# Kernel tuning notes

Hardware: AMD Instinct MI355X
Metric: run time of the kernel (lower is better)

The kernel has to match this reference:

```python
import jax, jax.numpy as jnp
import numpy as np
from jax.ops import segment_sum

N_V = 50000   # vertices
N_E = 10000   # hyperedges
N_P = 800000  # incidence pairs
D_IN = 256
D_OUT = 256
NEG_SLOPE = 0.01


def setup_inputs() -> dict:
    key = jax.random.key(0)
    k1, k2, k3, k4, k5 = jax.random.split(key, 5)
    X = jax.random.normal(k1, (N_V, D_IN), dtype=jnp.float32)
    W = jax.random.normal(k2, (D_IN, D_OUT), dtype=jnp.float32) * (1.0 / np.sqrt(D_IN))
    b = jax.random.normal(k3, (D_OUT,), dtype=jnp.float32) * 0.01
    v_idx = jax.random.randint(k4, (N_P,), 0, N_V, dtype=jnp.int32)
    e_idx = jax.random.randint(k5, (N_P,), 0, N_E, dtype=jnp.int32)
    return {"X": X, "W": W, "b": b, "v_idx": v_idx, "e_idx": e_idx,
            "num_hyperedges": N_E}


def _mean_scatter(msg, idx, num_segments):
    # segment mean with count clamped to >=1 (empty segments -> 0)
    s = segment_sum(msg, idx, num_segments=num_segments)
    cnt = segment_sum(jnp.ones((msg.shape[0],), msg.dtype), idx,
                      num_segments=num_segments)
    return s / jnp.maximum(cnt, 1.0)[:, None]


def reference(X, W, b, v_idx, e_idx, num_hyperedges):
    # theta: linear projection  [N_V, D_OUT]
    H = X @ W + b
    # v2e mean: hyperedge features from member vertices
    e_feat = _mean_scatter(H[v_idx], e_idx, num_hyperedges)   # [N_E, D_OUT]
    # e2v mean: vertex features from incident hyperedges
    v_feat = _mean_scatter(e_feat[e_idx], v_idx, X.shape[0])  # [N_V, D_OUT]
    # leaky relu, default negative slope 0.01
    return jnp.where(v_feat >= 0, v_feat, NEG_SLOPE * v_feat)
```

## Files before the change

kernel.cpp:

```cpp
#include <hip/hip_runtime.h>

#define D 256
#define NEG_SLOPE 0.01f
#define E_PAD 192
#define V_PAD 64
#define EB 32
#define VB 64
#define NBE 313
#define NBV 782
#define CAP_E 3328
#define CAP_V 1536
#define CHUNK 4096
#define NS 8
#define DS 32

__device__ __forceinline__ unsigned short f2bf(float f) {
    union { float f; unsigned u; } x; x.f = f;
    unsigned r = x.u + 0x7fffu + ((x.u >> 16) & 1u);
    return (unsigned short)(r >> 16);
}
__device__ __forceinline__ float bf2f(unsigned short h) {
    union { float f; unsigned u; } x; x.u = ((unsigned)h) << 16;
    return x.f;
}

__global__ __launch_bounds__(256) void prep_kernel(
        const float* __restrict__ X, unsigned short* __restrict__ Xhs,
        const int* __restrict__ v_idx, const int* __restrict__ e_idx,
        int* __restrict__ bc_e, int* __restrict__ bc_v,
        unsigned* __restrict__ pe, unsigned* __restrict__ pv,
        int n_v, int n_p, int gp) {
    __shared__ int he[NBE], hv[NBV], beb[NBE], bvb[NBV];
    const int tid = threadIdx.x;
    if ((int)blockIdx.x < gp) {
        const int base = (int)blockIdx.x * CHUNK;
        for (int i = tid; i < NBE; i += 256) he[i] = 0;
        for (int i = tid; i < NBV; i += 256) hv[i] = 0;
        __syncthreads();
        #pragma unroll 4
        for (int r = 0; r < CHUNK / 256; ++r) {
            int p = base + r * 256 + tid;
            if (p < n_p) {
                atomicAdd(&he[e_idx[p] >> 5], 1);
                atomicAdd(&hv[v_idx[p] >> 6], 1);
            }
        }
        __syncthreads();
        for (int b = tid; b < NBE; b += 256) {
            int c = he[b];
            beb[b] = c ? atomicAdd(&bc_e[b], c) : 0;
            he[b] = 0;
        }
        for (int b = tid; b < NBV; b += 256) {
            int c = hv[b];
            bvb[b] = c ? atomicAdd(&bc_v[b], c) : 0;
            hv[b] = 0;
        }
        __syncthreads();
        #pragma unroll 4
        for (int r = 0; r < CHUNK / 256; ++r) {
            int p = base + r * 256 + tid;
            if (p < n_p) {
                int e = e_idx[p], v = v_idx[p];
                int b1 = e >> 5;
                int s1 = beb[b1] + atomicAdd(&he[b1], 1);
                if (s1 < CAP_E) pe[(size_t)b1 * CAP_E + s1] = (unsigned)v | ((unsigned)e << 16);
                int b2 = v >> 6;
                int s2 = bvb[b2] + atomicAdd(&hv[b2], 1);
                if (s2 < CAP_V) pv[(size_t)b2 * CAP_V + s2] = (unsigned)e | ((unsigned)v << 16);
            }
        }
    } else {
        int i = ((int)blockIdx.x - gp) * 256 + tid;
        if (i >= n_v * 64) return;
        int v = i >> 6;
        int d4 = (i & 63) * 4;
        float4 val = *(const float4*)(X + (size_t)v * D + d4);
        ushort4 h;
        h.x = f2bf(val.x); h.y = f2bf(val.y); h.z = f2bf(val.z); h.w = f2bf(val.w);
        int s = d4 >> 5, wd = d4 & 31;
        *(ushort4*)(Xhs + (size_t)s * n_v * DS + (size_t)v * DS + wd) = h;
    }
}

__global__ __launch_bounds__(256) void build_kernel(
        const unsigned* __restrict__ pe, const unsigned* __restrict__ pv,
        const int* __restrict__ bc_e, const int* __restrict__ bc_v,
        unsigned short* __restrict__ e_adj, int* __restrict__ e_fill,
        unsigned short* __restrict__ v_adj, int* __restrict__ v_fill,
        int n_e, int n_v) {
    __shared__ unsigned short adj[EB * E_PAD];
    __shared__ int cnt[VB];
    const int tid = threadIdx.x;
    if ((int)blockIdx.x < NBE) {
        const int b = blockIdx.x;
        const int e0 = b * EB;
        int m = n_e - e0; if (m > EB) m = EB;
        for (int i = tid; i < EB; i += 256) cnt[i] = 0;
        __syncthreads();
        int total = bc_e[b]; if (total > CAP_E) total = CAP_E;
        for (int i = tid; i < total; i += 256) {
            unsigned p = pe[(size_t)b * CAP_E + i];
            int v = (int)(p & 0xFFFFu);
            int el = (int)(p >> 16) - e0;
            int s = atomicAdd(&cnt[el], 1);
            if (s < E_PAD) adj[el * E_PAD + s] = (unsigned short)v;
        }
        __syncthreads();
        unsigned* gout = (unsigned*)(e_adj + (size_t)e0 * E_PAD);
        const unsigned* lin = (const unsigned*)adj;
        int words = m * E_PAD / 2;
        for (int j = tid; j < words; j += 256) gout[j] = lin[j];
        for (int el = tid; el < m; el += 256) {
            int c = cnt[el]; if (c > E_PAD) c = E_PAD;
            e_fill[e0 + el] = c;
        }
    } else {
        const int b = (int)blockIdx.x - NBE;
        const int v0 = b * VB;
        int m = n_v - v0; if (m > VB) m = VB;
        for (int i = tid; i < VB; i += 256) cnt[i] = 0;
        __syncthreads();
        int total = bc_v[b]; if (total > CAP_V) total = CAP_V;
        for (int i = tid; i < total; i += 256) {
            unsigned p = pv[(size_t)b * CAP_V + i];
            int e = (int)(p & 0xFFFFu);
            int vl = (int)(p >> 16) - v0;
            int s = atomicAdd(&cnt[vl], 1);
            if (s < V_PAD) adj[vl * V_PAD + s] = (unsigned short)e;
        }
        __syncthreads();
        unsigned* gout = (unsigned*)(v_adj + (size_t)v0 * V_PAD);
        const unsigned* lin = (const unsigned*)adj;
        int words = m * V_PAD / 2;
        for (int j = tid; j < words; j += 256) gout[j] = lin[j];
        for (int vl = tid; vl < m; vl += 256) {
            int c = cnt[vl]; if (c > V_PAD) c = V_PAD;
            v_fill[v0 + vl] = c;
        }
    }
}

__global__ __launch_bounds__(256) void v2e_kernel(
        const unsigned short* __restrict__ Xhs, const int* __restrict__ e_fill,
        const unsigned short* __restrict__ e_adj, float* __restrict__ Xagg,
        int n_e, int n_v) {
    const int s   = blockIdx.x;
    const int grp = threadIdx.x >> 3;
    const int sub = threadIdx.x & 7;
    const int e   = blockIdx.y * 32 + grp;
    if (e >= n_e) return;
    const unsigned short* tab = Xhs + (size_t)s * n_v * DS + (sub << 2);
    const unsigned short* adj = e_adj + (size_t)e * E_PAD;
    int cnt = e_fill[e]; if (cnt > E_PAD) cnt = E_PAD;
    float ax = 0.f, ay = 0.f, az = 0.f, aw = 0.f;
    int i = 0;
    for (; i + 8 <= cnt; i += 8) {
        ushort4 A0 = *(const ushort4*)(adj + i);
        ushort4 A1 = *(const ushort4*)(adj + i + 4);
        ushort4 a0 = *(const ushort4*)(tab + (size_t)A0.x * DS);
        ushort4 a1 = *(const ushort4*)(tab + (size_t)A0.y * DS);
        ushort4 a2 = *(const ushort4*)(tab + (size_t)A0.z * DS);
        ushort4 a3 = *(const ushort4*)(tab + (size_t)A0.w * DS);
        ushort4 a4 = *(const ushort4*)(tab + (size_t)A1.x * DS);
        ushort4 a5 = *(const ushort4*)(tab + (size_t)A1.y * DS);
        ushort4 a6 = *(const ushort4*)(tab + (size_t)A1.z * DS);
        ushort4 a7 = *(const ushort4*)(tab + (size_t)A1.w * DS);
        ax += (bf2f(a0.x) + bf2f(a1.x)) + (bf2f(a2.x) + bf2f(a3.x))
            + (bf2f(a4.x) + bf2f(a5.x)) + (bf2f(a6.x) + bf2f(a7.x));
        ay += (bf2f(a0.y) + bf2f(a1.y)) + (bf2f(a2.y) + bf2f(a3.y))
            + (bf2f(a4.y) + bf2f(a5.y)) + (bf2f(a6.y) + bf2f(a7.y));
        az += (bf2f(a0.z) + bf2f(a1.z)) + (bf2f(a2.z) + bf2f(a3.z))
            + (bf2f(a4.z) + bf2f(a5.z)) + (bf2f(a6.z) + bf2f(a7.z));
        aw += (bf2f(a0.w) + bf2f(a1.w)) + (bf2f(a2.w) + bf2f(a3.w))
            + (bf2f(a4.w) + bf2f(a5.w)) + (bf2f(a6.w) + bf2f(a7.w));
    }
    for (; i < cnt; ++i) {
        int v = adj[i];
        ushort4 a = *(const ushort4*)(tab + (size_t)v * DS);
        ax += bf2f(a.x); ay += bf2f(a.y); az += bf2f(a.z); aw += bf2f(a.w);
    }
    int c = cnt < 1 ? 1 : cnt;
    float inv = 1.0f / (float)c;
    float4 o;
    o.x = ax * inv; o.y = ay * inv; o.z = az * inv; o.w = aw * inv;
    *(float4*)(Xagg + (size_t)e * D + s * DS + (sub << 2)) = o;
}

#define BM 64
#define BN 64
#define BK 64
#define SAK 68
#define SBN 68

__global__ __launch_bounds__(256) void gemm_kernel(
        const float* __restrict__ A, const float* __restrict__ B,
        const float* __restrict__ bias, const int* __restrict__ e_cnt,
        unsigned short* __restrict__ Ehs, int M) {
    __shared__ float As[BM * SAK];
    __shared__ float Bs[BK * SBN];
    const int tid = threadIdx.x;
    const int tx = tid & 15, ty = tid >> 4;
    const int m0 = blockIdx.y * BM;
    const int n0 = blockIdx.x * BN;

    float acc[4][4] = {};

    for (int k0 = 0; k0 < D; k0 += BK) {
        #pragma unroll
        for (int r = 0; r < 4; ++r) {
            int l  = (tid + r * 256) * 4;
            int am = l >> 6;
            int ak = l & 63;
            int grow = m0 + am;
            float4 v = make_float4(0.f, 0.f, 0.f, 0.f);
            if (grow < M) v = *(const float4*)(A + (size_t)grow * D + k0 + ak);
            *(float4*)(&As[am * SAK + ak]) = v;
        }
        #pragma unroll
        for (int r = 0; r < 4; ++r) {
            int l  = (tid + r * 256) * 4;
            int bk = l >> 6;
            int bn = l & 63;
            float4 v = *(const float4*)(B + (size_t)(k0 + bk) * D + n0 + bn);
            *(float4*)(&Bs[bk * SBN + bn]) = v;
        }
        __syncthreads();

        #pragma unroll 8
        for (int kk = 0; kk < BK; ++kk) {
            float a0 = As[(ty * 4 + 0) * SAK + kk];
            float a1 = As[(ty * 4 + 1) * SAK + kk];
            float a2 = As[(ty * 4 + 2) * SAK + kk];
            float a3 = As[(ty * 4 + 3) * SAK + kk];
            float4 bv = *(const float4*)(Bs + kk * SBN + tx * 4);
            acc[0][0] += a0 * bv.x; acc[0][1] += a0 * bv.y; acc[0][2] += a0 * bv.z; acc[0][3] += a0 * bv.w;
            acc[1][0] += a1 * bv.x; acc[1][1] += a1 * bv.y; acc[1][2] += a1 * bv.z; acc[1][3] += a1 * bv.w;
            acc[2][0] += a2 * bv.x; acc[2][1] += a2 * bv.y; acc[2][2] += a2 * bv.z; acc[2][3] += a2 * bv.w;
            acc[3][0] += a3 * bv.x; acc[3][1] += a3 * bv.y; acc[3][2] += a3 * bv.z; acc[3][3] += a3 * bv.w;
        }
        __syncthreads();
    }

    float4 bb = *(const float4*)(bias + n0 + tx * 4);
    const int dcol = n0 + tx * 4;
    const int ss = dcol >> 5, wd = dcol & 31;
    #pragma unroll
    for (int i = 0; i < 4; ++i) {
        int row = m0 + ty * 4 + i;
        if (row < M) {
            bool nonempty = e_cnt[row] > 0;
            ushort4 o;
            o.x = f2bf(nonempty ? acc[i][0] + bb.x : 0.f);
            o.y = f2bf(nonempty ? acc[i][1] + bb.y : 0.f);
            o.z = f2bf(nonempty ? acc[i][2] + bb.z : 0.f);
            o.w = f2bf(nonempty ? acc[i][3] + bb.w : 0.f);
            *(ushort4*)(Ehs + (size_t)ss * M * DS + (size_t)row * DS + wd) = o;
        }
    }
}

__global__ __launch_bounds__(256) void e2v_kernel(
        const unsigned short* __restrict__ Ehs, const unsigned short* __restrict__ v_adj,
        const int* __restrict__ v_fill, float* __restrict__ out, int n_v, int n_e) {
    const int s   = blockIdx.x;
    const int grp = threadIdx.x >> 3;
    const int sub = threadIdx.x & 7;
    const int v   = blockIdx.y * 32 + grp;
    if (v >= n_v) return;
    const unsigned short* tab = Ehs + (size_t)s * n_e * DS + (sub << 2);
    const unsigned short* a = v_adj + (size_t)v * V_PAD;
    int c = v_fill[v]; if (c > V_PAD) c = V_PAD;
    float ax = 0.f, ay = 0.f, az = 0.f, aw = 0.f;
    int i = 0;
    for (; i + 8 <= c; i += 8) {
        ushort4 E0 = *(const ushort4*)(a + i);
        ushort4 E1 = *(const ushort4*)(a + i + 4);
        ushort4 a0 = *(const ushort4*)(tab + (size_t)E0.x * DS);
        ushort4 a1 = *(const ushort4*)(tab + (size_t)E0.y * DS);
        ushort4 a2 = *(const ushort4*)(tab + (size_t)E0.z * DS);
        ushort4 a3 = *(const ushort4*)(tab + (size_t)E0.w * DS);
        ushort4 a4 = *(const ushort4*)(tab + (size_t)E1.x * DS);
        ushort4 a5 = *(const ushort4*)(tab + (size_t)E1.y * DS);
        ushort4 a6 = *(const ushort4*)(tab + (size_t)E1.z * DS);
        ushort4 a7 = *(const ushort4*)(tab + (size_t)E1.w * DS);
        ax += (bf2f(a0.x) + bf2f(a1.x)) + (bf2f(a2.x) + bf2f(a3.x))
            + (bf2f(a4.x) + bf2f(a5.x)) + (bf2f(a6.x) + bf2f(a7.x));
        ay += (bf2f(a0.y) + bf2f(a1.y)) + (bf2f(a2.y) + bf2f(a3.y))
            + (bf2f(a4.y) + bf2f(a5.y)) + (bf2f(a6.y) + bf2f(a7.y));
        az += (bf2f(a0.z) + bf2f(a1.z)) + (bf2f(a2.z) + bf2f(a3.z))
            + (bf2f(a4.z) + bf2f(a5.z)) + (bf2f(a6.z) + bf2f(a7.z));
        aw += (bf2f(a0.w) + bf2f(a1.w)) + (bf2f(a2.w) + bf2f(a3.w))
            + (bf2f(a4.w) + bf2f(a5.w)) + (bf2f(a6.w) + bf2f(a7.w));
    }
    for (; i < c; ++i) {
        int e = a[i];
        ushort4 x = *(const ushort4*)(tab + (size_t)e * DS);
        ax += bf2f(x.x); ay += bf2f(x.y); az += bf2f(x.z); aw += bf2f(x.w);
    }
    int cc = c < 1 ? 1 : c;
    float inv = 1.0f / (float)cc;
    ax *= inv; ay *= inv; az *= inv; aw *= inv;
    float4 o;
    o.x = ax >= 0.f ? ax : NEG_SLOPE * ax;
    o.y = ay >= 0.f ? ay : NEG_SLOPE * ay;
    o.z = az >= 0.f ? az : NEG_SLOPE * az;
    o.w = aw >= 0.f ? aw : NEG_SLOPE * aw;
    *(float4*)(out + (size_t)v * D + s * DS + (sub << 2)) = o;
}

extern "C" void kernel_launch(void* const* d_in, const int* in_sizes, int n_in,
                              void* d_out, int out_size, void* d_ws, size_t ws_size,
                              hipStream_t stream) {
    const float* X    = (const float*)d_in[0];
    const float* W    = (const float*)d_in[1];
    const float* bias = (const float*)d_in[2];
    const int* v_idx  = (const int*)d_in[3];
    const int* e_idx  = (const int*)d_in[4];
    const int n_v = in_sizes[0] / D;
    const int n_p = in_sizes[3];
    const int n_e = 10000;

    char* w = (char*)d_ws;
    size_t off = 0;
    auto alloc = [&](size_t bytes) -> void* {
        void* p = w + off;
        off = (off + bytes + 255) & ~(size_t)255;
        return p;
    };
    unsigned short* Xhs = (unsigned short*)alloc((size_t)NS * n_v * DS * sizeof(unsigned short));
    float* Xagg         = (float*)alloc((size_t)n_e * D * sizeof(float));
    unsigned short* Ehs = (unsigned short*)alloc((size_t)n_e * D * sizeof(unsigned short));
    unsigned short* e_adj = (unsigned short*)alloc((size_t)n_e * E_PAD * sizeof(unsigned short));
    unsigned short* v_adj = (unsigned short*)alloc((size_t)n_v * V_PAD * sizeof(unsigned short));
    unsigned* pe   = (unsigned*)alloc((size_t)NBE * CAP_E * sizeof(unsigned));
    unsigned* pv   = (unsigned*)alloc((size_t)NBV * CAP_V * sizeof(unsigned));
    int* fills     = (int*)alloc((size_t)(n_e + n_v) * sizeof(int));
    int* e_fill = fills;
    int* v_fill = fills + n_e;
    int* bc        = (int*)alloc((size_t)(NBE + NBV) * sizeof(int));
    int* bc_e = bc;
    int* bc_v = bc + NBE;

    hipMemsetAsync(bc, 0, (size_t)(NBE + NBV) * sizeof(int), stream);

    int gp = (n_p + CHUNK - 1) / CHUNK;
    int gc = (n_v * 64 + 255) / 256;
    prep_kernel<<<gp + gc, 256, 0, stream>>>(X, Xhs, v_idx, e_idx,
                                             bc_e, bc_v, pe, pv, n_v, n_p, gp);

    build_kernel<<<NBE + NBV, 256, 0, stream>>>(pe, pv, bc_e, bc_v,
                                                e_adj, e_fill, v_adj, v_fill,
                                                n_e, n_v);

    dim3 vgrid(NS, (n_e + 31) / 32);
    v2e_kernel<<<vgrid, 256, 0, stream>>>(Xhs, e_fill, e_adj, Xagg, n_e, n_v);

    dim3 ggrid(D / BN, (n_e + BM - 1) / BM);
    gemm_kernel<<<ggrid, 256, 0, stream>>>(Xagg, W, bias, e_fill, Ehs, n_e);

    dim3 egrid(NS, (n_v + 31) / 32);
    e2v_kernel<<<egrid, 256, 0, stream>>>(Ehs, v_adj, v_fill, (float*)d_out, n_v, n_e);
}
```

Before: 260.9 us.

## Widen gather loads to 16 bytes and repack edge table into 128-wide slices

Both gather kernels now load 8 bf16 values per thread as a uint4 and unpack them with shifts and masks, instead of 4 values via ushort4. v2e keeps 8 slices of 32 columns but uses 4 threads per edge. The edge-feature table written by the GEMM is repacked into 2 slices of 128 columns, so e2v uses 16 threads per vertex and re-reads each vertex's adjacency list only twice instead of 8 times. The aim is fewer, wider memory transactions and less redundant index traffic. The cost is fewer threads per row and coarser column slices, which may reduce cache locality of the hyperedge table.

```diff
diff --git a/kernel.cpp b/kernel.cpp
--- a/kernel.cpp
+++ b/kernel.cpp
@@ -13,15 +13,24 @@
 #define CHUNK 4096
 #define NS 8
 #define DS 32
+#define NSE 2
+#define DSE 128
 
 __device__ __forceinline__ unsigned short f2bf(float f) {
     union { float f; unsigned u; } x; x.f = f;
     unsigned r = x.u + 0x7fffu + ((x.u >> 16) & 1u);
     return (unsigned short)(r >> 16);
 }
-__device__ __forceinline__ float bf2f(unsigned short h) {
-    union { float f; unsigned u; } x; x.u = ((unsigned)h) << 16;
-    return x.f;
+__device__ __forceinline__ void acc8(float* acc, uint4 g) {
+    union { unsigned u; float f; } t;
+    t.u = g.x << 16;         acc[0] += t.f;
+    t.u = g.x & 0xffff0000u; acc[1] += t.f;
+    t.u = g.y << 16;         acc[2] += t.f;
+    t.u = g.y & 0xffff0000u; acc[3] += t.f;
+    t.u = g.z << 16;         acc[4] += t.f;
+    t.u = g.z & 0xffff0000u; acc[5] += t.f;
+    t.u = g.w << 16;         acc[6] += t.f;
+    t.u = g.w & 0xffff0000u; acc[7] += t.f;
 }
 
 __global__ __launch_bounds__(256) void prep_kernel(
@@ -146,45 +155,41 @@
         const unsigned short* __restrict__ e_adj, float* __restrict__ Xagg,
         int n_e, int n_v) {
     const int s   = blockIdx.x;
-    const int grp = threadIdx.x >> 3;
-    const int sub = threadIdx.x & 7;
-    const int e   = blockIdx.y * 32 + grp;
+    const int grp = threadIdx.x >> 2;
+    const int sub = threadIdx.x & 3;
+    const int e   = blockIdx.y * 64 + grp;
     if (e >= n_e) return;
-    const unsigned short* tab = Xhs + (size_t)s * n_v * DS + (sub << 2);
+    const unsigned short* tab = Xhs + (size_t)s * n_v * DS + (sub << 3);
     const unsigned short* adj = e_adj + (size_t)e * E_PAD;
     int cnt = e_fill[e]; if (cnt > E_PAD) cnt = E_PAD;
-    float ax = 0.f, ay = 0.f, az = 0.f, aw = 0.f;
+    float acc[8] = {};
     int i = 0;
     for (; i + 8 <= cnt; i += 8) {
         ushort4 A0 = *(const ushort4*)(adj + i);
         ushort4 A1 = *(const ushort4*)(adj + i + 4);
-        ushort4 a0 = *(const ushort4*)(tab + (size_t)A0.x * DS);
-        ushort4 a1 = *(const ushort4*)(tab + (size_t)A0.y * DS);
-        ushort4 a2 = *(const ushort4*)(tab + (size_t)A0.z * DS);
-        ushort4 a3 = *(const ushort4*)(tab + (size_t)A0.w * DS);
-        ushort4 a4 = *(const ushort4*)(tab + (size_t)A1.x * DS);
-        ushort4 a5 = *(const ushort4*)(tab + (size_t)A1.y * DS);
-        ushort4 a6 = *(const ushort4*)(tab + (size_t)A1.z * DS);
-        ushort4 a7 = *(const ushort4*)(tab + (size_t)A1.w * DS);
-        ax += (bf2f(a0.x) + bf2f(a1.x)) + (bf2f(a2.x) + bf2f(a3.x))
-            + (bf2f(a4.x) + bf2f(a5.x)) + (bf2f(a6.x) + bf2f(a7.x));
-        ay += (bf2f(a0.y) + bf2f(a1.y)) + (bf2f(a2.y) + bf2f(a3.y))
-            + (bf2f(a4.y) + bf2f(a5.y)) + (bf2f(a6.y) + bf2f(a7.y));
-        az += (bf2f(a0.z) + bf2f(a1.z)) + (bf2f(a2.z) + bf2f(a3.z))
-            + (bf2f(a4.z) + bf2f(a5.z)) + (bf2f(a6.z) + bf2f(a7.z));
-        aw += (bf2f(a0.w) + bf2f(a1.w)) + (bf2f(a2.w) + bf2f(a3.w))
-            + (bf2f(a4.w) + bf2f(a5.w)) + (bf2f(a6.w) + bf2f(a7.w));
+        uint4 g0 = *(const uint4*)(tab + (size_t)A0.x * DS);
+        uint4 g1 = *(const uint4*)(tab + (size_t)A0.y * DS);
+        uint4 g2 = *(const uint4*)(tab + (size_t)A0.z * DS);
+        uint4 g3 = *(const uint4*)(tab + (size_t)A0.w * DS);
+        uint4 g4 = *(const uint4*)(tab + (size_t)A1.x * DS);
+        uint4 g5 = *(const uint4*)(tab + (size_t)A1.y * DS);
+        uint4 g6 = *(const uint4*)(tab + (size_t)A1.z * DS);
+        uint4 g7 = *(const uint4*)(tab + (size_t)A1.w * DS);
+        acc8(acc, g0); acc8(acc, g1); acc8(acc, g2); acc8(acc, g3);
+        acc8(acc, g4); acc8(acc, g5); acc8(acc, g6); acc8(acc, g7);
     }
     for (; i < cnt; ++i) {
-        int v = adj[i];
-        ushort4 a = *(const ushort4*)(tab + (size_t)v * DS);
-        ax += bf2f(a.x); ay += bf2f(a.y); az += bf2f(a.z); aw += bf2f(a.w);
+        uint4 g = *(const uint4*)(tab + (size_t)adj[i] * DS);
+        acc8(acc, g);
     }
     int c = cnt < 1 ? 1 : cnt;
     float inv = 1.0f / (float)c;
-    float4 o;
-    o.x = ax * inv; o.y = ay * inv; o.z = az * inv; o.w = aw * inv;
-    *(float4*)(Xagg + (size_t)e * D + s * DS + (sub << 2)) = o;
+    float4 o0, o1;
+    o0.x = acc[0] * inv; o0.y = acc[1] * inv; o0.z = acc[2] * inv; o0.w = acc[3] * inv;
+    o1.x = acc[4] * inv; o1.y = acc[5] * inv; o1.z = acc[6] * inv; o1.w = acc[7] * inv;
+    float* orow = Xagg + (size_t)e * D + s * DS + (sub << 3);
+    *(float4*)(orow)     = o0;
+    *(float4*)(orow + 4) = o1;
 }
 
 #define BM 64
@@ -244,7 +249,7 @@
 
     float4 bb = *(const float4*)(bias + n0 + tx * 4);
     const int dcol = n0 + tx * 4;
-    const int ss = dcol >> 5, wd = dcol & 31;
+    const int ss = dcol >> 7, wd = dcol & 127;
     #pragma unroll
     for (int i = 0; i < 4; ++i) {
         int row = m0 + ty * 4 + i;
@@ -255,7 +260,7 @@
             o.y = f2bf(nonempty ? acc[i][1] + bb.y : 0.f);
             o.z = f2bf(nonempty ? acc[i][2] + bb.z : 0.f);
             o.w = f2bf(nonempty ? acc[i][3] + bb.w : 0.f);
-            *(ushort4*)(Ehs + (size_t)ss * M * DS + (size_t)row * DS + wd) = o;
+            *(ushort4*)(Ehs + (size_t)ss * M * DSE + (size_t)row * DSE + wd) = o;
         }
     }
 }
@@ -264,49 +269,49 @@
         const unsigned short* __restrict__ Ehs, const unsigned short* __restrict__ v_adj,
         const int* __restrict__ v_fill, float* __restrict__ out, int n_v, int n_e) {
     const int s   = blockIdx.x;
-    const int grp = threadIdx.x >> 3;
-    const int sub = threadIdx.x & 7;
-    const int v   = blockIdx.y * 32 + grp;
+    const int grp = threadIdx.x >> 4;
+    const int sub = threadIdx.x & 15;
+    const int v   = blockIdx.y * 16 + grp;
     if (v >= n_v) return;
-    const unsigned short* tab = Ehs + (size_t)s * n_e * DS + (sub << 2);
-    const unsigned short* a = v_adj + (size_t)v * V_PAD;
+    const unsigned short* tab = Ehs + (size_t)s * n_e * DSE + (sub << 3);
+    const unsigned short* a   = v_adj + (size_t)v * V_PAD;
     int c = v_fill[v]; if (c > V_PAD) c = V_PAD;
-    float ax = 0.f, ay = 0.f, az = 0.f, aw = 0.f;
+    float acc[8] = {};
     int i = 0;
     for (; i + 8 <= c; i += 8) {
         ushort4 E0 = *(const ushort4*)(a + i);
         ushort4 E1 = *(const ushort4*)(a + i + 4);
-        ushort4 a0 = *(const ushort4*)(tab + (size_t)E0.x * DS);
-        ushort4 a1 = *(const ushort4*)(tab + (size_t)E0.y * DS);
-        ushort4 a2 = *(const ushort4*)(tab + (size_t)E0.z * DS);
-        ushort4 a3 = *(const ushort4*)(tab + (size_t)E0.w * DS);
-        ushort4 a4 = *(const ushort4*)(tab + (size_t)E1.x * DS);
-        ushort4 a5 = *(const ushort4*)(tab + (size_t)E1.y * DS);
-        ushort4 a6 = *(const ushort4*)(tab + (size_t)E1.z * DS);
-        ushort4 a7 = *(const ushort4*)(tab + (size_t)E1.w * DS);
-        ax += (bf2f(a0.x) + bf2f(a1.x)) + (bf2f(a2.x) + bf2f(a3.x))
-            + (bf2f(a4.x) + bf2f(a5.x)) + (bf2f(a6.x) + bf2f(a7.x));
-        ay += (bf2f(a0.y) + bf2f(a1.y)) + (bf2f(a2.y) + bf2f(a3.y))
-            + (bf2f(a4.y) + bf2f(a5.y)) + (bf2f(a6.y) + bf2f(a7.y));
-        az += (bf2f(a0.z) + bf2f(a1.z)) + (bf2f(a2.z) + bf2f(a3.z))
-            + (bf2f(a4.z) + bf2f(a5.z)) + (bf2f(a6.z) + bf2f(a7.z));
-        aw += (bf2f(a0.w) + bf2f(a1.w)) + (bf2f(a2.w) + bf2f(a3.w))
-            + (bf2f(a4.w) + bf2f(a5.w)) + (bf2f(a6.w) + bf2f(a7.w));
+        uint4 g0 = *(const uint4*)(tab + (size_t)E0.x * DSE);
+        uint4 g1 = *(const uint4*)(tab + (size_t)E0.y * DSE);
+        uint4 g2 = *(const uint4*)(tab + (size_t)E0.z * DSE);
+        uint4 g3 = *(const uint4*)(tab + (size_t)E0.w * DSE);
+        uint4 g4 = *(const uint4*)(tab + (size_t)E1.x * DSE);
+        uint4 g5 = *(const uint4*)(tab + (size_t)E1.y * DSE);
+        uint4 g6 = *(const uint4*)(tab + (size_t)E1.z * DSE);
+        uint4 g7 = *(const uint4*)(tab + (size_t)E1.w * DSE);
+        acc8(acc, g0); acc8(acc, g1); acc8(acc, g2); acc8(acc, g3);
+        acc8(acc, g4); acc8(acc, g5); acc8(acc, g6); acc8(acc, g7);
     }
     for (; i < c; ++i) {
-        int e = a[i];
-        ushort4 x = *(const ushort4*)(tab + (size_t)e * DS);
-        ax += bf2f(x.x); ay += bf2f(x.y); az += bf2f(x.z); aw += bf2f(x.w);
+        uint4 g = *(const uint4*)(tab + (size_t)a[i] * DSE);
+        acc8(acc, g);
     }
     int cc = c < 1 ? 1 : c;
     float inv = 1.0f / (float)cc;
-    ax *= inv; ay *= inv; az *= inv; aw *= inv;
-    float4 o;
-    o.x = ax >= 0.f ? ax : NEG_SLOPE * ax;
-    o.y = ay >= 0.f ? ay : NEG_SLOPE * ay;
-    o.z = az >= 0.f ? az : NEG_SLOPE * az;
-    o.w = aw >= 0.f ? aw : NEG_SLOPE * aw;
-    *(float4*)(out + (size_t)v * D + s * DS + (sub << 2)) = o;
+    float4 o0, o1;
+    #pragma unroll
+    for (int k = 0; k < 8; ++k) acc[k] *= inv;
+    o0.x = acc[0] >= 0.f ? acc[0] : NEG_SLOPE * acc[0];
+    o0.y = acc[1] >= 0.f ? acc[1] : NEG_SLOPE * acc[1];
+    o0.z = acc[2] >= 0.f ? acc[2] : NEG_SLOPE * acc[2];
+    o0.w = acc[3] >= 0.f ? acc[3] : NEG_SLOPE * acc[3];
+    o1.x = acc[4] >= 0.f ? acc[4] : NEG_SLOPE * acc[4];
+    o1.y = acc[5] >= 0.f ? acc[5] : NEG_SLOPE * acc[5];
+    o1.z = acc[6] >= 0.f ? acc[6] : NEG_SLOPE * acc[6];
+    o1.w = acc[7] >= 0.f ? acc[7] : NEG_SLOPE * acc[7];
+    float* orow = out + (size_t)v * D + s * DSE + (sub << 3);
+    *(float4*)(orow)     = o0;
+    *(float4*)(orow + 4) = o1;
 }
 
 extern "C" void kernel_launch(void* const* d_in, const int* in_sizes, int n_in,
@@ -353,12 +358,12 @@
                                                 e_adj, e_fill, v_adj, v_fill,
                                                 n_e, n_v);
 
-    dim3 vgrid(NS, (n_e + 31) / 32);
+    dim3 vgrid(NS, (n_e + 63) / 64);
     v2e_kernel<<<vgrid, 256, 0, stream>>>(Xhs, e_fill, e_adj, Xagg, n_e, n_v);
 
     dim3 ggrid(D / BN, (n_e + BM - 1) / BM);
     gemm_kernel<<<ggrid, 256, 0, stream>>>(Xagg, W, bias, e_fill, Ehs, n_e);
 
-    dim3 egrid(NS, (n_v + 31) / 32);
+    dim3 egrid(NSE, (n_v + 15) / 16);
     e2v_kernel<<<egrid, 256, 0, stream>>>(Ehs, v_adj, v_fill, (float*)d_out, n_v, n_e);
 }
```

Result: faster. 243.6 us (-6.7%).
